# Kernel optimization log

Hardware: AMD Instinct MI355X
Metric: run time of the kernel (lower is better)

## Reference

```python
import jax, jax.numpy as jnp
import numpy as np

B, C, N, F_IN = 8, 5, 512, 768
H, D_HID, D_OUT = 4, 128, 64
NEG_SLOPE = 0.2


def _gat_layer(h, mask, W, a_l, a_r, b, apply_relu):
    # h: [B,N,Fin], mask: [B,N,N] bool (mask[b,i,j]=True means edge i->j)
    Bn, Nn, _ = h.shape
    Hh, Dd = a_l.shape
    feat = (h @ W).reshape(Bn, Nn, Hh, Dd)              # [B,N,H,D]
    el = jnp.einsum('bnhd,hd->bnh', feat, a_l)          # src scores
    er = jnp.einsum('bnhd,hd->bnh', feat, a_r)          # dst scores
    e = jax.nn.leaky_relu(el[:, :, None, :] + er[:, None, :, :], NEG_SLOPE)  # [B,src,dst,H]
    m = mask[..., None]
    e = jnp.where(m, e, jnp.finfo(e.dtype).min)
    emax = jnp.max(e, axis=1, keepdims=True)
    p = jnp.where(m, jnp.exp(e - emax), 0.0)
    s = jnp.sum(p, axis=1, keepdims=True)
    alpha = p / jnp.maximum(s, 1e-9)                    # edge softmax over incoming edges per dst
    out = jnp.einsum('bijh,bihd->bjhd', alpha, feat)    # aggregate src features to dst
    out = out + b.reshape(1, 1, Hh, Dd)
    if apply_relu:
        out = jax.nn.relu(out)
    return out                                           # [B,N,H,D]


def setup_inputs() -> dict:
    key = jax.random.key(0)
    ks = jax.random.split(key, 16)
    x = jax.random.normal(ks[0], (B, C, N, F_IN), dtype=jnp.float32)
    adj = (jax.random.uniform(ks[1], (B, C, N, N)) < 0.1).astype(jnp.float32)
    node_nums = jnp.full((B,), N, dtype=jnp.int32)
    s = 0.02
    W0 = jax.random.normal(ks[2], (C, F_IN, H * D_HID)) * s
    al0 = jax.random.normal(ks[3], (C, H, D_HID)) * s
    ar0 = jax.random.normal(ks[4], (C, H, D_HID)) * s
    b0 = jnp.zeros((C, H * D_HID), jnp.float32)
    W1 = jax.random.normal(ks[5], (C, H * D_HID, H * D_HID)) * s
    al1 = jax.random.normal(ks[6], (C, H, D_HID)) * s
    ar1 = jax.random.normal(ks[7], (C, H, D_HID)) * s
    b1 = jnp.zeros((C, H * D_HID), jnp.float32)
    W2 = jax.random.normal(ks[8], (C, H * D_HID, H * D_OUT)) * s
    al2 = jax.random.normal(ks[9], (C, H, D_OUT)) * s
    ar2 = jax.random.normal(ks[10], (C, H, D_OUT)) * s
    b2 = jnp.zeros((C, H * D_OUT), jnp.float32)
    return dict(x=x, adj=adj, W0=W0, al0=al0, ar0=ar0, b0=b0,
                W1=W1, al1=al1, ar1=ar1, b1=b1,
                W2=W2, al2=al2, ar2=ar2, b2=b2, node_nums=node_nums)


def reference(x, adj, W0, al0, ar0, b0, W1, al1, ar1, b1, W2, al2, ar2, b2, node_nums):
    # Original concatenates per-batch node slices and takes channel 0 features only.
    h0 = x[:, 0]                       # [B,N,F_IN]
    logits_all = []
    for c in range(C):
        mask = adj[:, c] > 0           # [B,N,N]
        h = _gat_layer(h0, mask, W0[c], al0[c], ar0[c], b0[c].reshape(H, D_HID), True).reshape(B, N, H * D_HID)
        h = _gat_layer(h, mask, W1[c], al1[c], ar1[c], b1[c].reshape(H, D_HID), True).reshape(B, N, H * D_HID)
        out = _gat_layer(h, mask, W2[c], al2[c], ar2[c], b2[c].reshape(H, D_OUT), False).mean(axis=2)  # [B,N,D_OUT]
        logits_all.append(out)
    return jnp.concatenate(logits_all, axis=-1)  # [B,N,C*D_OUT]
```

## Files before the change

### kernel.cpp

```cpp
#include <hip/hip_runtime.h>

typedef unsigned int uint;
typedef unsigned short ushort_t;
typedef __attribute__((ext_vector_type(8))) short short8;
typedef __attribute__((ext_vector_type(4))) float f32x4;

#define NB 8
#define NC 5
#define NN 512
#define FIN 768
#define NH 4
#define MT 4096

__device__ __forceinline__ float b2f(ushort_t u){ uint x = ((uint)u)<<16; return __builtin_bit_cast(float, x); }
__device__ __forceinline__ ushort_t f2b(float f){
  uint u = __builtin_bit_cast(uint, f);
  u += 0x7FFFu + ((u>>16)&1u);
  return (ushort_t)(u>>16);
}
__device__ __forceinline__ ushort_t f2b_fast(float f){
  uint u = __builtin_bit_cast(uint, f);
  return (ushort_t)((u + 0x8000u)>>16);
}

#if __has_builtin(__builtin_amdgcn_cvt_pk_bf16_f32)
typedef __bf16 bf16x2 __attribute__((ext_vector_type(2)));
__device__ __forceinline__ uint pk2(float a, float b){
  return __builtin_bit_cast(uint, __builtin_amdgcn_cvt_pk_bf16_f32(a, b));
}
#else
__device__ __forceinline__ uint pk2(float a, float b){
  return (uint)f2b_fast(a) | ((uint)f2b_fast(b) << 16);
}
#endif

#define GLL16(gp, lp) __builtin_amdgcn_global_load_lds( \
    (const __attribute__((address_space(1))) void*)(gp), \
    (__attribute__((address_space(3))) void*)(lp), 16, 0, 0)

__global__ __launch_bounds__(256) void prep(const float* __restrict__ x, ushort_t* __restrict__ h0b,
                                            const float* __restrict__ W0, ushort_t* __restrict__ Wt0,
                                            const float* __restrict__ W1, ushort_t* __restrict__ Wt1,
                                            const float* __restrict__ W2, ushort_t* __restrict__ Wt2,
                                            const float* __restrict__ adj, uint* __restrict__ adjB,
                                            float* __restrict__ dout){
  __shared__ float tile[32][33];
  int bid = blockIdx.x, t = threadIdx.x;
  if (bid < 3072){
    int tid = bid*256 + t;
    int row = tid/192, q = tid%192;
    int b = row >> 9, n = row & 511;
    float4 v = *(const float4*)(x + ((size_t)(b*NC)*NN + n)*FIN + q*4);
    ushort4 o; o.x = f2b(v.x); o.y = f2b(v.y); o.z = f2b(v.z); o.w = f2b(v.w);
    *(ushort4*)(h0b + (size_t)row*FIN + q*4) = o;
  } else if (bid < 6912){
    const float* W; ushort_t* Wt; int K, N, c, x0, y0;
    if (bid < 4992){ int l = bid-3072; K=768; N=512; W=W0; Wt=Wt0; c=l/384; int r=l%384; x0=r%16; y0=r/16; }
    else if (bid < 6272){ int l = bid-4992; K=512; N=512; W=W1; Wt=Wt1; c=l/256; int r=l%256; x0=r%16; y0=r/16; }
    else { int l = bid-6272; K=512; N=256; W=W2; Wt=Wt2; c=l/128; int r=l%128; x0=r%8; y0=r/8; }
    int n0 = x0*32, k0 = y0*32;
    int tx = t & 31, ty = t >> 5;
    const float* Wp = W + (size_t)c*K*N;
    ushort_t* Wtp = Wt + (size_t)c*K*N;
    #pragma unroll
    for (int r=0;r<4;r++) tile[ty+r*8][tx] = Wp[(size_t)(k0+ty+r*8)*N + n0+tx];
    __syncthreads();
    #pragma unroll
    for (int r=0;r<4;r++) Wtp[(size_t)(n0+ty+r*8)*K + k0+tx] = f2b(tile[tx][ty+r*8]);
  } else if (bid < 7552){
    int l = bid - 6912;
    int iw = l & 15, zz = l >> 4;
    const float* ap = adj + (size_t)zz*NN*NN + (size_t)iw*32*NN;
    uint w0 = 0, w1 = 0;
    #pragma unroll 8
    for (int q=0;q<32;q++){
      if (ap[(size_t)q*NN + t]       > 0.f) w0 |= (1u<<q);
      if (ap[(size_t)q*NN + t + 256] > 0.f) w1 |= (1u<<q);
    }
    adjB[((size_t)zz*16 + iw)*512 + t]       = w0;
    adjB[((size_t)zz*16 + iw)*512 + t + 256] = w1;
  } else {
    int l = bid - 7552;
    float4 z = {0.f,0.f,0.f,0.f};
    float4* dp = (float4*)dout + (size_t)l*512;
    dp[t] = z; dp[t+256] = z;
  }
}

template<int DH>
__global__ __launch_bounds__(256) void gemm_tn(const ushort_t* __restrict__ A,
                                               const ushort_t* __restrict__ Bt,
                                               ushort_t* __restrict__ Ob,
                                               const float* __restrict__ al, const float* __restrict__ ar,
                                               float* __restrict__ el, float* __restrict__ E1, float* __restrict__ E2,
                                               float* __restrict__ er, float* __restrict__ R1, float* __restrict__ R2,
                                               int K, long a_cs, long b_cs){
  constexpr int DT = NH*DH;
  __shared__ __align__(16) char smem[128*136*2];
  __shared__ float als_s[128], ars_s[128];
  ushort_t* As = (ushort_t*)smem;
  ushort_t* Bs = As + 128*32;
  ushort_t* St = (ushort_t*)smem;
  int c = blockIdx.z;
  const ushort_t* Ap = A + (size_t)c*a_cs;
  const ushort_t* Bp = Bt + (size_t)c*b_cs;
  int m0 = blockIdx.y*128, n0 = blockIdx.x*128;
  int t = threadIdx.x, lane = t & 63, w = t >> 6;
  int l15 = lane & 15, quad = lane >> 4;
  int wm = (w & 1)*64, wn = (w >> 1)*64;
  if (t < 128){
    als_s[t] = al[(size_t)c*NH*DH + n0 + t];
    ars_s[t] = ar[(size_t)c*NH*DH + n0 + t];
  }
  f32x4 acc[4][4] = {};
  for (int k0 = 0; k0 < K; k0 += 32){
    __syncthreads();
    {
      int i = t;
      GLL16(Ap + (size_t)(m0 + (i>>2))*K + k0 + (i&3)*8, As + (size_t)(w*64)*8);
      GLL16(Bp + (size_t)(n0 + (i>>2))*K + k0 + (i&3)*8, Bs + (size_t)(w*64)*8);
      i = t + 256;
      GLL16(Ap + (size_t)(m0 + (i>>2))*K + k0 + (i&3)*8, As + (size_t)(w*64 + 256)*8);
      GLL16(Bp + (size_t)(n0 + (i>>2))*K + k0 + (i&3)*8, Bs + (size_t)(w*64 + 256)*8);
    }
    __syncthreads();
    short8 af[4], bfr[4];
    #pragma unroll
    for (int im=0; im<4; im++) af[im] = *(const short8*)(As + (size_t)(wm + im*16 + l15)*32 + quad*8);
    #pragma unroll
    for (int in=0; in<4; in++) bfr[in] = *(const short8*)(Bs + (size_t)(wn + in*16 + l15)*32 + quad*8);
    #pragma unroll
    for (int im=0; im<4; im++)
      #pragma unroll
      for (int in=0; in<4; in++)
        acc[im][in] = __builtin_amdgcn_mfma_f32_16x16x32_bf16(af[im], bfr[in], acc[im][in], 0, 0, 0);
  }
  __syncthreads();
  #pragma unroll
  for (int im=0; im<4; im++)
    #pragma unroll
    for (int in=0; in<4; in++){
      int n = wn + in*16 + l15;
      #pragma unroll
      for (int r=0; r<4; r++){
        int m = wm + im*16 + quad*4 + r;
        St[(size_t)n*136 + m] = f2b(acc[im][in][r]);
      }
    }
  __syncthreads();
  {
    int n_loc = t >> 1, half = t & 1;
    const ushort_t* srcp = St + (size_t)n_loc*136 + half*64;
    ushort_t* dstc = Ob + (size_t)c*MT*DT;
    #pragma unroll
    for (int q=0;q<8;q++){
      size_t g = (size_t)(m0>>3) + half*8 + q;
      *(short8*)(dstc + (g*DT + n0 + n_loc)*8) = *(const short8*)(srcp + q*8);
    }
  }
  {
    int m = t >> 1, half = t & 1;
    float sl = 0.f, sr = 0.f;
    const ushort_t* stp = St + (size_t)(half*64)*136 + m;
    #pragma unroll 8
    for (int nn=0; nn<64; nn++){
      float f = b2f(stp[(size_t)nn*136]);
      int n = half*64 + nn;
      sl += f*als_s[n]; sr += f*ars_s[n];
    }
    size_t base = (size_t)c*NH*MT;
    if (DH == 128){
      sl += __shfl_xor(sl, 1); sr += __shfl_xor(sr, 1);
      size_t idx = base + (size_t)(n0>>7)*MT + m0 + m;
      if (half == 0){ el[idx]=sl; E1[idx]=__expf(sl); E2[idx]=__expf(0.2f*sl); }
      else          { er[idx]=sr; R1[idx]=__expf(sr); R2[idx]=__expf(0.2f*sr); }
    } else {
      size_t idx = base + (size_t)((n0>>6)+half)*MT + m0 + m;
      el[idx]=sl; E1[idx]=__expf(sl); E2[idx]=__expf(0.2f*sl);
      er[idx]=sr; R1[idx]=__expf(sr); R2[idx]=__expf(0.2f*sr);
    }
  }
}

template<int DH, int RELU, int FINAL>
__global__ __launch_bounds__(256,3) void agg(const ushort_t* __restrict__ featB,
                                             const uint* __restrict__ adjB,
                                             const float* __restrict__ el, const float* __restrict__ E1,
                                             const float* __restrict__ E2,
                                             const float* __restrict__ er, const float* __restrict__ R1,
                                             const float* __restrict__ R2,
                                             const float* __restrict__ bias,
                                             ushort_t* __restrict__ outp,
                                             float* __restrict__ dout){
  constexpr int DT = NH*DH;
  constexpr int BN = DH/16;
  constexpr int CELLS = 32768/(DH*16);
  constexpr int STAGES = 64/CELLS;
  constexpr int STEPS = CELLS/4;
  constexpr int PARTS = (DH*8)/512;
  __shared__ __align__(16) ushort_t Fs[CELLS*DH*8];
  __shared__ float el_s[512], E1_s[512], E2_s[512];
  __shared__ uint Ms[16*64];
  int bid = blockIdx.x;
  int g = bid % 160, jt = bid / 160;
  int c = g>>5, b = (g>>2)&7, h = g&3;
  int zz = b*NC + c;
  int j0 = jt*64;
  int t = threadIdx.x, lane = t&63, w = t>>6, l15 = lane&15, quad = lane>>4;
  size_t eb = (size_t)(c*NH + h)*MT + b*NN;
  const ushort_t* fBc = featB + ((size_t)(c*512 + b*64)*DT + h*DH)*8;
  el_s[t] = el[eb + t]; el_s[t+256] = el[eb + t+256];
  E1_s[t] = E1[eb + t]; E1_s[t+256] = E1[eb + t+256];
  E2_s[t] = E2[eb + t]; E2_s[t+256] = E2[eb + t+256];
  #pragma unroll
  for (int k=0;k<4;k++){
    int idx = k*256 + t;
    Ms[idx] = adjB[((size_t)zz*16 + (idx>>6))*512 + j0 + (idx&63)];
  }
  int jme = j0 + w*16 + l15;
  float erv = er[eb + jme];
  float R1v = R1[eb + jme];
  float R2v = R2[eb + jme];
  short8 onesv;
  #pragma unroll
  for (int q=0;q<8;q++) onesv[q] = (short)0x3F80;
  f32x4 acc[BN] = {};
  f32x4 accs = {0.f,0.f,0.f,0.f};
  for (int sg = 0; sg < STAGES; sg++){
    __syncthreads();
    #pragma unroll
    for (int u = 0; u < CELLS/4; u++){
      int cell = w*(CELLS/4) + u;
      #pragma unroll
      for (int part = 0; part < PARTS; part++)
        GLL16(fBc + (size_t)(sg*CELLS + cell)*DT*8 + part*512 + lane*8,
              Fs + (size_t)cell*(DH*8) + part*512);
    }
    __syncthreads();
    #pragma unroll
    for (int st = 0; st < STEPS; st++){
      int i0c = sg*(CELLS*8) + st*32;
      uint mby = (Ms[(i0c>>5)*64 + w*16 + l15] >> (quad*8)) & 0xFFu;
      float4 ea  = *(const float4*)&el_s[i0c + quad*8];
      float4 eb4 = *(const float4*)&el_s[i0c + quad*8 + 4];
      float4 x1a = *(const float4*)&E1_s[i0c + quad*8];
      float4 x1b = *(const float4*)&E1_s[i0c + quad*8 + 4];
      float4 x2a = *(const float4*)&E2_s[i0c + quad*8];
      float4 x2b = *(const float4*)&E2_s[i0c + quad*8 + 4];
      float ev[8]  = {ea.x,ea.y,ea.z,ea.w,eb4.x,eb4.y,eb4.z,eb4.w};
      float e1v[8] = {x1a.x,x1a.y,x1a.z,x1a.w,x1b.x,x1b.y,x1b.z,x1b.w};
      float e2v[8] = {x2a.x,x2a.y,x2a.z,x2a.w,x2b.x,x2b.y,x2b.z,x2b.w};
      float pv[8];
      #pragma unroll
      for (int q=0;q<8;q++){
        float s  = ev[q] + erv;
        float Ei = (s > 0.f) ? e1v[q] : e2v[q];
        float Rv = (s > 0.f) ? R1v : R2v;
        float p  = Ei*Rv;
        pv[q] = ((mby>>q)&1u) ? p : 0.f;
      }
      uint4 pw;
      pw.x = pk2(pv[0], pv[1]); pw.y = pk2(pv[2], pv[3]);
      pw.z = pk2(pv[4], pv[5]); pw.w = pk2(pv[6], pv[7]);
      short8 af = __builtin_bit_cast(short8, pw);
      accs = __builtin_amdgcn_mfma_f32_16x16x32_bf16(af, onesv, accs, 0, 0, 0);
      #pragma unroll
      for (int half=0; half<2; half++){
        short8 bfr[BN/2];
        #pragma unroll
        for (int in=0; in<BN/2; in++)
          bfr[in] = *(const short8*)&Fs[(size_t)(st*4+quad)*(DH*8) + ((half*(BN/2)+in)*16 + l15)*8];
        #pragma unroll
        for (int in=0; in<BN/2; in++)
          acc[half*(BN/2)+in] = __builtin_amdgcn_mfma_f32_16x16x32_bf16(af, bfr[in], acc[half*(BN/2)+in], 0, 0, 0);
      }
    }
  }
  float bv[BN];
  #pragma unroll
  for (int in=0; in<BN; in++) bv[in] = bias[(size_t)c*DT + h*DH + in*16 + l15];
  if (!FINAL){
    ushort_t* op = outp + ((size_t)c*MT + b*NN + j0 + w*16)*DT + h*DH;
    #pragma unroll
    for (int r=0; r<4; r++){
      int jr = quad*4 + r;
      float sinv = 1.f / fmaxf(accs[r], 1e-9f);
      #pragma unroll
      for (int in=0; in<BN; in++){
        float o = acc[in][r]*sinv + bv[in];
        if (RELU) o = fmaxf(o, 0.f);
        op[(size_t)jr*DT + in*16 + l15] = f2b_fast(o);
      }
    }
  } else {
    float* dp = dout + ((size_t)b*NN + j0 + w*16)*(NC*64) + c*64;
    #pragma unroll
    for (int r=0; r<4; r++){
      int jr = quad*4 + r;
      float sinv = 1.f / fmaxf(accs[r], 1e-9f);
      #pragma unroll
      for (int in=0; in<BN; in++){
        float o = acc[in][r]*sinv + bv[in];
        atomicAdd(dp + (size_t)jr*(NC*64) + in*16 + l15, 0.25f*o);
      }
    }
  }
}

extern "C" void kernel_launch(void* const* d_in, const int* in_sizes, int n_in,
                              void* d_out, int out_size, void* d_ws, size_t ws_size,
                              hipStream_t stream){
  const float* x   = (const float*)d_in[0];
  const float* adj = (const float*)d_in[1];
  const float* W0  = (const float*)d_in[2];
  const float* al0 = (const float*)d_in[3];
  const float* ar0 = (const float*)d_in[4];
  const float* b0  = (const float*)d_in[5];
  const float* W1  = (const float*)d_in[6];
  const float* al1 = (const float*)d_in[7];
  const float* ar1 = (const float*)d_in[8];
  const float* b1  = (const float*)d_in[9];
  const float* W2  = (const float*)d_in[10];
  const float* al2 = (const float*)d_in[11];
  const float* ar2 = (const float*)d_in[12];
  const float* b2  = (const float*)d_in[13];

  ushort_t* h0b  = (ushort_t*)d_ws;
  ushort_t* Wt0  = h0b  + (size_t)MT*FIN;
  ushort_t* Wt1  = Wt0  + (size_t)5*512*768;
  ushort_t* Wt2  = Wt1  + (size_t)5*512*512;
  ushort_t* featB= Wt2  + (size_t)5*256*512;
  ushort_t* hnat = featB+ (size_t)5*(size_t)MT*512;
  uint*     adjB = (uint*)(hnat + (size_t)5*(size_t)MT*512);
  float*    elp  = (float*)(adjB + (size_t)40*16*512);
  float*    E1p  = elp + (size_t)NC*NH*MT;
  float*    E2p  = E1p + (size_t)NC*NH*MT;
  float*    erp  = E2p + (size_t)NC*NH*MT;
  float*    R1p  = erp + (size_t)NC*NH*MT;
  float*    R2p  = R1p + (size_t)NC*NH*MT;
  float*    dout = (float*)d_out;

  prep<<<8192, 256, 0, stream>>>(x, h0b, W0, Wt0, W1, Wt1, W2, Wt2, adj, adjB, dout);

  gemm_tn<128><<<dim3(4,32,5), 256, 0, stream>>>(h0b, Wt0, featB, al0, ar0,
                                                 elp, E1p, E2p, erp, R1p, R2p,
                                                 768, 0L, (long)512*768);
  agg<128,1,0><<<1280, 256, 0, stream>>>(featB, adjB, elp, E1p, E2p, erp, R1p, R2p, b0, hnat, dout);
  gemm_tn<128><<<dim3(4,32,5), 256, 0, stream>>>(hnat, Wt1, featB, al1, ar1,
                                                 elp, E1p, E2p, erp, R1p, R2p,
                                                 512, (long)MT*512, (long)512*512);
  agg<128,1,0><<<1280, 256, 0, stream>>>(featB, adjB, elp, E1p, E2p, erp, R1p, R2p, b1, hnat, dout);
  gemm_tn<64><<<dim3(2,32,5), 256, 0, stream>>>(hnat, Wt2, featB, al2, ar2,
                                                elp, E1p, E2p, erp, R1p, R2p,
                                                512, (long)MT*512, (long)256*512);
  agg<64,0,1><<<1280, 256, 0, stream>>>(featB, adjB, elp, E1p, E2p, erp, R1p, R2p, b2, hnat, dout);
}
```

Measured before the change: 321.3 us.

## Halve GEMM M-tile and double-buffer feature tiles in aggregation kernel

The projection GEMM now uses 64x128 tiles instead of 128x128, doubling the grid and shrinking shared memory so more blocks fit per CU. The epilogue's attention-score reduction is reworked to four partial sums combined with shuffles. The aggregation kernel replaces its staged load-then-compute loop with a two-buffer prefetch, loading the next 32-row chunk of features while computing the current one, and raises the occupancy hint. The aim is more parallelism and overlap of global loads with MFMA work, at the cost of less operand reuse per GEMM tile and an extra barrier per aggregation step.

```diff
diff --git a/kernel.cpp b/kernel.cpp
--- a/kernel.cpp
+++ b/kernel.cpp
@@ -88,102 +88,99 @@
 }
 
 template<int DH>
-__global__ __launch_bounds__(256) void gemm_tn(const ushort_t* __restrict__ A,
-                                               const ushort_t* __restrict__ Bt,
-                                               ushort_t* __restrict__ Ob,
-                                               const float* __restrict__ al, const float* __restrict__ ar,
-                                               float* __restrict__ el, float* __restrict__ E1, float* __restrict__ E2,
-                                               float* __restrict__ er, float* __restrict__ R1, float* __restrict__ R2,
-                                               int K, long a_cs, long b_cs){
+__global__ __launch_bounds__(256,5) void gemm_tn(const ushort_t* __restrict__ A,
+                                                 const ushort_t* __restrict__ Bt,
+                                                 ushort_t* __restrict__ Ob,
+                                                 const float* __restrict__ al, const float* __restrict__ ar,
+                                                 float* __restrict__ el, float* __restrict__ E1, float* __restrict__ E2,
+                                                 float* __restrict__ er, float* __restrict__ R1, float* __restrict__ R2,
+                                                 int K, long a_cs, long b_cs){
   constexpr int DT = NH*DH;
-  __shared__ __align__(16) char smem[128*136*2];
+  __shared__ __align__(16) char smem[128*72*2];
   __shared__ float als_s[128], ars_s[128];
   ushort_t* As = (ushort_t*)smem;
-  ushort_t* Bs = As + 128*32;
+  ushort_t* Bs = As + 64*32;
   ushort_t* St = (ushort_t*)smem;
   int c = blockIdx.z;
   const ushort_t* Ap = A + (size_t)c*a_cs;
   const ushort_t* Bp = Bt + (size_t)c*b_cs;
-  int m0 = blockIdx.y*128, n0 = blockIdx.x*128;
+  int m0 = blockIdx.y*64, n0 = blockIdx.x*128;
   int t = threadIdx.x, lane = t & 63, w = t >> 6;
   int l15 = lane & 15, quad = lane >> 4;
-  int wm = (w & 1)*64, wn = (w >> 1)*64;
+  int wm = (w & 1)*32, wn = (w >> 1)*64;
   if (t < 128){
     als_s[t] = al[(size_t)c*NH*DH + n0 + t];
     ars_s[t] = ar[(size_t)c*NH*DH + n0 + t];
   }
-  f32x4 acc[4][4] = {};
+  f32x4 acc[2][4] = {};
   for (int k0 = 0; k0 < K; k0 += 32){
     __syncthreads();
-    {
-      int i = t;
-      GLL16(Ap + (size_t)(m0 + (i>>2))*K + k0 + (i&3)*8, As + (size_t)(w*64)*8);
-      GLL16(Bp + (size_t)(n0 + (i>>2))*K + k0 + (i&3)*8, Bs + (size_t)(w*64)*8);
-      i = t + 256;
-      GLL16(Ap + (size_t)(m0 + (i>>2))*K + k0 + (i&3)*8, As + (size_t)(w*64 + 256)*8);
-      GLL16(Bp + (size_t)(n0 + (i>>2))*K + k0 + (i&3)*8, Bs + (size_t)(w*64 + 256)*8);
-    }
+    GLL16(Ap + (size_t)(m0 + w*16 + (lane>>2))*K + k0 + (lane&3)*8, As + (size_t)(w*16)*32);
+    GLL16(Bp + (size_t)(n0 + w*16 + (lane>>2))*K + k0 + (lane&3)*8, Bs + (size_t)(w*16)*32);
+    GLL16(Bp + (size_t)(n0 + 64 + w*16 + (lane>>2))*K + k0 + (lane&3)*8, Bs + (size_t)(64 + w*16)*32);
     __syncthreads();
-    short8 af[4], bfr[4];
-    #pragma unroll
-    for (int im=0; im<4; im++) af[im] = *(const short8*)(As + (size_t)(wm + im*16 + l15)*32 + quad*8);
+    short8 af[2], bfr[4];
+    #pragma unroll
+    for (int im=0; im<2; im++) af[im] = *(const short8*)(As + (size_t)(wm + im*16 + l15)*32 + quad*8);
     #pragma unroll
     for (int in=0; in<4; in++) bfr[in] = *(const short8*)(Bs + (size_t)(wn + in*16 + l15)*32 + quad*8);
     #pragma unroll
-    for (int im=0; im<4; im++)
+    for (int im=0; im<2; im++)
       #pragma unroll
       for (int in=0; in<4; in++)
         acc[im][in] = __builtin_amdgcn_mfma_f32_16x16x32_bf16(af[im], bfr[in], acc[im][in], 0, 0, 0);
   }
   __syncthreads();
   #pragma unroll
-  for (int im=0; im<4; im++)
+  for (int im=0; im<2; im++)
     #pragma unroll
     for (int in=0; in<4; in++){
       int n = wn + in*16 + l15;
       #pragma unroll
       for (int r=0; r<4; r++){
         int m = wm + im*16 + quad*4 + r;
-        St[(size_t)n*136 + m] = f2b(acc[im][in][r]);
+        St[(size_t)n*72 + m] = f2b(acc[im][in][r]);
       }
     }
   __syncthreads();
   {
     int n_loc = t >> 1, half = t & 1;
-    const ushort_t* srcp = St + (size_t)n_loc*136 + half*64;
+    const ushort_t* srcp = St + (size_t)n_loc*72 + half*32;
     ushort_t* dstc = Ob + (size_t)c*MT*DT;
     #pragma unroll
-    for (int q=0;q<8;q++){
-      size_t g = (size_t)(m0>>3) + half*8 + q;
+    for (int q=0;q<4;q++){
+      size_t g = (size_t)(m0>>3) + half*4 + q;
       *(short8*)(dstc + (g*DT + n0 + n_loc)*8) = *(const short8*)(srcp + q*8);
     }
   }
   {
-    int m = t >> 1, half = t & 1;
+    int m = t >> 2, part = t & 3;
     float sl = 0.f, sr = 0.f;
-    const ushort_t* stp = St + (size_t)(half*64)*136 + m;
+    const ushort_t* stp = St + (size_t)(part*32)*72 + m;
     #pragma unroll 8
-    for (int nn=0; nn<64; nn++){
-      float f = b2f(stp[(size_t)nn*136]);
-      int n = half*64 + nn;
+    for (int nn=0; nn<32; nn++){
+      float f = b2f(stp[(size_t)nn*72]);
+      int n = part*32 + nn;
       sl += f*als_s[n]; sr += f*ars_s[n];
     }
+    sl += __shfl_xor(sl, 1); sr += __shfl_xor(sr, 1);
     size_t base = (size_t)c*NH*MT;
     if (DH == 128){
-      sl += __shfl_xor(sl, 1); sr += __shfl_xor(sr, 1);
+      sl += __shfl_xor(sl, 2); sr += __shfl_xor(sr, 2);
       size_t idx = base + (size_t)(n0>>7)*MT + m0 + m;
-      if (half == 0){ el[idx]=sl; E1[idx]=__expf(sl); E2[idx]=__expf(0.2f*sl); }
-      else          { er[idx]=sr; R1[idx]=__expf(sr); R2[idx]=__expf(0.2f*sr); }
+      if (part == 0){ el[idx]=sl; E1[idx]=__expf(sl); E2[idx]=__expf(0.2f*sl); }
+      else if (part == 1){ er[idx]=sr; R1[idx]=__expf(sr); R2[idx]=__expf(0.2f*sr); }
     } else {
-      size_t idx = base + (size_t)((n0>>6)+half)*MT + m0 + m;
-      el[idx]=sl; E1[idx]=__expf(sl); E2[idx]=__expf(0.2f*sl);
-      er[idx]=sr; R1[idx]=__expf(sr); R2[idx]=__expf(0.2f*sr);
+      int head = (n0>>6) + (part>>1);
+      size_t idx = base + (size_t)head*MT + m0 + m;
+      if ((part & 1) == 0){ el[idx]=sl; E1[idx]=__expf(sl); E2[idx]=__expf(0.2f*sl); }
+      else                { er[idx]=sr; R1[idx]=__expf(sr); R2[idx]=__expf(0.2f*sr); }
     }
   }
 }
 
 template<int DH, int RELU, int FINAL>
-__global__ __launch_bounds__(256,3) void agg(const ushort_t* __restrict__ featB,
+__global__ __launch_bounds__(256,5) void agg(const ushort_t* __restrict__ featB,
                                              const uint* __restrict__ adjB,
                                              const float* __restrict__ el, const float* __restrict__ E1,
                                              const float* __restrict__ E2,
@@ -194,11 +191,7 @@
                                              float* __restrict__ dout){
   constexpr int DT = NH*DH;
   constexpr int BN = DH/16;
-  constexpr int CELLS = 32768/(DH*16);
-  constexpr int STAGES = 64/CELLS;
-  constexpr int STEPS = CELLS/4;
-  constexpr int PARTS = (DH*8)/512;
-  __shared__ __align__(16) ushort_t Fs[CELLS*DH*8];
+  __shared__ __align__(16) ushort_t Fs[2][4*DH*8];
   __shared__ float el_s[512], E1_s[512], E2_s[512];
   __shared__ uint Ms[16*64];
   int bid = blockIdx.x;
@@ -226,55 +219,53 @@
   for (int q=0;q<8;q++) onesv[q] = (short)0x3F80;
   f32x4 acc[BN] = {};
   f32x4 accs = {0.f,0.f,0.f,0.f};
-  for (int sg = 0; sg < STAGES; sg++){
+  #pragma unroll
+  for (int part=0; part<DH/64; part++)
+    GLL16(fBc + (size_t)w*DT*8 + part*512 + lane*8, &Fs[0][w*(DH*8) + part*512]);
+  __syncthreads();
+  for (int ic = 0; ic < 16; ic++){
+    int buf = ic & 1;
+    if (ic < 15){
+      #pragma unroll
+      for (int part=0; part<DH/64; part++)
+        GLL16(fBc + (size_t)((ic+1)*4+w)*DT*8 + part*512 + lane*8, &Fs[buf^1][w*(DH*8) + part*512]);
+    }
+    int i0c = ic*32;
+    uint mby = (Ms[ic*64 + w*16 + l15] >> (quad*8)) & 0xFFu;
+    float4 ea  = *(const float4*)&el_s[i0c + quad*8];
+    float4 eb4 = *(const float4*)&el_s[i0c + quad*8 + 4];
+    float4 x1a = *(const float4*)&E1_s[i0c + quad*8];
+    float4 x1b = *(const float4*)&E1_s[i0c + quad*8 + 4];
+    float4 x2a = *(const float4*)&E2_s[i0c + quad*8];
+    float4 x2b = *(const float4*)&E2_s[i0c + quad*8 + 4];
+    float ev[8]  = {ea.x,ea.y,ea.z,ea.w,eb4.x,eb4.y,eb4.z,eb4.w};
+    float e1v[8] = {x1a.x,x1a.y,x1a.z,x1a.w,x1b.x,x1b.y,x1b.z,x1b.w};
+    float e2v[8] = {x2a.x,x2a.y,x2a.z,x2a.w,x2b.x,x2b.y,x2b.z,x2b.w};
+    float pv[8];
+    #pragma unroll
+    for (int q=0;q<8;q++){
+      float s  = ev[q] + erv;
+      float Ei = (s > 0.f) ? e1v[q] : e2v[q];
+      float Rv = (s > 0.f) ? R1v : R2v;
+      float p  = Ei*Rv;
+      pv[q] = ((mby>>q)&1u) ? p : 0.f;
+    }
+    uint4 pw;
+    pw.x = pk2(pv[0], pv[1]); pw.y = pk2(pv[2], pv[3]);
+    pw.z = pk2(pv[4], pv[5]); pw.w = pk2(pv[6], pv[7]);
+    short8 af = __builtin_bit_cast(short8, pw);
+    accs = __builtin_amdgcn_mfma_f32_16x16x32_bf16(af, onesv, accs, 0, 0, 0);
+    #pragma unroll
+    for (int half=0; half<2; half++){
+      short8 bfr[BN/2];
+      #pragma unroll
+      for (int in=0; in<BN/2; in++)
+        bfr[in] = *(const short8*)&Fs[buf][quad*(DH*8) + ((half*(BN/2)+in)*16 + l15)*8];
+      #pragma unroll
+      for (int in=0; in<BN/2; in++)
+        acc[half*(BN/2)+in] = __builtin_amdgcn_mfma_f32_16x16x32_bf16(af, bfr[in], acc[half*(BN/2)+in], 0, 0, 0);
+    }
     __syncthreads();
-    #pragma unroll
-    for (int u = 0; u < CELLS/4; u++){
-      int cell = w*(CELLS/4) + u;
-      #pragma unroll
-      for (int part = 0; part < PARTS; part++)
-        GLL16(fBc + (size_t)(sg*CELLS + cell)*DT*8 + part*512 + lane*8,
-              Fs + (size_t)cell*(DH*8) + part*512);
-    }
-    __syncthreads();
-    #pragma unroll
-    for (int st = 0; st < STEPS; st++){
-      int i0c = sg*(CELLS*8) + st*32;
-      uint mby = (Ms[(i0c>>5)*64 + w*16 + l15] >> (quad*8)) & 0xFFu;
-      float4 ea  = *(const float4*)&el_s[i0c + quad*8];
-      float4 eb4 = *(const float4*)&el_s[i0c + quad*8 + 4];
-      float4 x1a = *(const float4*)&E1_s[i0c + quad*8];
-      float4 x1b = *(const float4*)&E1_s[i0c + quad*8 + 4];
-      float4 x2a = *(const float4*)&E2_s[i0c + quad*8];
-      float4 x2b = *(const float4*)&E2_s[i0c + quad*8 + 4];
-      float ev[8]  = {ea.x,ea.y,ea.z,ea.w,eb4.x,eb4.y,eb4.z,eb4.w};
-      float e1v[8] = {x1a.x,x1a.y,x1a.z,x1a.w,x1b.x,x1b.y,x1b.z,x1b.w};
-      float e2v[8] = {x2a.x,x2a.y,x2a.z,x2a.w,x2b.x,x2b.y,x2b.z,x2b.w};
-      float pv[8];
-      #pragma unroll
-      for (int q=0;q<8;q++){
-        float s  = ev[q] + erv;
-        float Ei = (s > 0.f) ? e1v[q] : e2v[q];
-        float Rv = (s > 0.f) ? R1v : R2v;
-        float p  = Ei*Rv;
-        pv[q] = ((mby>>q)&1u) ? p : 0.f;
-      }
-      uint4 pw;
-      pw.x = pk2(pv[0], pv[1]); pw.y = pk2(pv[2], pv[3]);
-      pw.z = pk2(pv[4], pv[5]); pw.w = pk2(pv[6], pv[7]);
-      short8 af = __builtin_bit_cast(short8, pw);
-      accs = __builtin_amdgcn_mfma_f32_16x16x32_bf16(af, onesv, accs, 0, 0, 0);
-      #pragma unroll
-      for (int half=0; half<2; half++){
-        short8 bfr[BN/2];
-        #pragma unroll
-        for (int in=0; in<BN/2; in++)
-          bfr[in] = *(const short8*)&Fs[(size_t)(st*4+quad)*(DH*8) + ((half*(BN/2)+in)*16 + l15)*8];
-        #pragma unroll
-        for (int in=0; in<BN/2; in++)
-          acc[half*(BN/2)+in] = __builtin_amdgcn_mfma_f32_16x16x32_bf16(af, bfr[in], acc[half*(BN/2)+in], 0, 0, 0);
-      }
-    }
   }
   float bv[BN];
   #pragma unroll
@@ -342,15 +333,15 @@
 
   prep<<<8192, 256, 0, stream>>>(x, h0b, W0, Wt0, W1, Wt1, W2, Wt2, adj, adjB, dout);
 
-  gemm_tn<128><<<dim3(4,32,5), 256, 0, stream>>>(h0b, Wt0, featB, al0, ar0,
+  gemm_tn<128><<<dim3(4,64,5), 256, 0, stream>>>(h0b, Wt0, featB, al0, ar0,
                                                  elp, E1p, E2p, erp, R1p, R2p,
                                                  768, 0L, (long)512*768);
   agg<128,1,0><<<1280, 256, 0, stream>>>(featB, adjB, elp, E1p, E2p, erp, R1p, R2p, b0, hnat, dout);
-  gemm_tn<128><<<dim3(4,32,5), 256, 0, stream>>>(hnat, Wt1, featB, al1, ar1,
+  gemm_tn<128><<<dim3(4,64,5), 256, 0, stream>>>(hnat, Wt1, featB, al1, ar1,
                                                  elp, E1p, E2p, erp, R1p, R2p,
                                                  512, (long)MT*512, (long)512*512);
   agg<128,1,0><<<1280, 256, 0, stream>>>(featB, adjB, elp, E1p, E2p, erp, R1p, R2p, b1, hnat, dout);
-  gemm_tn<64><<<dim3(2,32,5), 256, 0, stream>>>(hnat, Wt2, featB, al2, ar2,
+  gemm_tn<64><<<dim3(2,64,5), 256, 0, stream>>>(hnat, Wt2, featB, al2, ar2,
                                                 elp, E1p, E2p, erp, R1p, R2p,
                                                 512, (long)MT*512, (long)256*512);
   agg<64,0,1><<<1280, 256, 0, stream>>>(featB, adjB, elp, E1p, E2p, erp, R1p, R2p, b2, hnat, dout);
```

Result: faster. 306.0 us (-4.8%).
